# Performance work log

Hardware: AMD Instinct MI355X
Metric: run time of the kernel (lower is better)

The kernel has to match this reference:

```python
import jax, jax.numpy as jnp
import numpy as np

INFINITY = 1000000000000.0
HEADS = 12
HEAD_SIZE = 64


def setup_inputs() -> dict:
    key = jax.random.key(0)
    k1, k2 = jax.random.split(key)
    B, S, H = 8, 512, 1024
    x = jax.random.normal(k1, (B, S, H), dtype=jnp.float32)
    mask = jnp.ones((B, S), dtype=jnp.float32)
    W = jax.random.normal(k2, (H, HEADS * HEAD_SIZE * 2), dtype=jnp.float32) * (1.0 / np.sqrt(H))
    b = jnp.zeros((HEADS * HEAD_SIZE * 2,), dtype=jnp.float32)
    return {"x": x, "mask": mask, "W": W, "b": b}


def _sinusoidal_pos(seq_len, dim, dtype):
    # pos[n, d] interleaved as [sin0, cos0, sin1, cos1, ...]
    position = jnp.arange(seq_len, dtype=dtype)  # (S,)
    indices = jnp.power(jnp.asarray(10000.0, dtype), -2.0 * jnp.arange(dim // 2, dtype=dtype) / dim)
    ang = position[:, None] * indices[None, :]  # (S, d/2)
    pos = jnp.stack([jnp.sin(ang), jnp.cos(ang)], axis=-1).reshape(seq_len, dim)
    return pos


def reference(x, mask, W, b):
    B, S, _ = x.shape
    hs = HEAD_SIZE
    proj = x @ W + b  # (B, S, HEADS*2*hs)
    proj = proj.reshape(B, S, HEADS, 2 * hs)
    qw, kw = proj[..., :hs], proj[..., hs:]  # (B, S, HEADS, hs)

    # RoPE (note: original uses torch .repeat, i.e. TILING, not interleave)
    pos = _sinusoidal_pos(S, hs, x.dtype)  # (S, hs)
    cos_half = pos[None, :, None, 1::2]  # (1, S, 1, hs/2)
    sin_half = pos[None, :, None, ::2]
    cos_pos = jnp.concatenate([cos_half, cos_half], axis=-1)  # tiled -> (1,S,1,hs)
    sin_pos = jnp.concatenate([sin_half, sin_half], axis=-1)

    def rotate(t):
        t2 = jnp.stack([-t[..., 1::2], t[..., ::2]], axis=-1).reshape(t.shape)
        return t * cos_pos + t2 * sin_pos

    qw = rotate(qw)
    kw = rotate(kw)

    logits = jnp.einsum('bmhd,bnhd->bhmn', qw, kw)  # (B, HEADS, S, S)

    # sequence masking on dim 2 (rows) and dim 3 (cols)
    m_row = mask[:, None, :, None]
    m_col = mask[:, None, None, :]
    logits = logits * m_row + (-INFINITY) * (1.0 - m_row)
    logits = logits * m_col + (-INFINITY) * (1.0 - m_col)

    # strictly-lower-triangular mask (exclude end < start)
    tri = jnp.tril(jnp.ones((S, S), dtype=logits.dtype), k=-1)
    logits = logits - tri * INFINITY
    return logits / (hs ** 0.5)
```

## Files before the change

kernel.cpp:

```cpp
#include <hip/hip_runtime.h>
#include <stdint.h>
#include <stddef.h>

#define NB 8
#define SS 512
#define HID 1024
#define NHEADS 12
#define HSZ 64
#define NPROJ 1536
#define MROWS 4096
#define NEG_INF 1000000000000.0f

typedef __attribute__((ext_vector_type(4))) float f32x4;
typedef __attribute__((ext_vector_type(8))) __bf16 bf16x8;
typedef __attribute__((ext_vector_type(4))) unsigned short us4;

typedef __attribute__((address_space(1))) unsigned char gu8;
typedef __attribute__((address_space(3))) unsigned char lu8;

static __device__ __forceinline__ void gld16(const void* g, void* l) {
  __builtin_amdgcn_global_load_lds((gu8*)(g), (lu8*)(l), 16, 0, 0);
}

static __device__ __forceinline__ unsigned short f2bf(float f) {
  union { float f; unsigned u; } x; x.f = f;
  unsigned r = x.u + 0x7fffu + ((x.u >> 16) & 1u);
  return (unsigned short)(r >> 16);
}

__global__ __launch_bounds__(256) void k_prep(
    const float4* __restrict__ x, const float* __restrict__ W,
    float2* __restrict__ tab, us4* __restrict__ xb, unsigned short* __restrict__ wbt) {
  __shared__ float t[32][33];
  const int bid = blockIdx.x;
  const int tid = threadIdx.x;
  if (bid < 64) {
    int tt = bid * 256 + tid;
    int s = tt >> 5, i = tt & 31;
    float rate = powf(10000.0f, -(float)i / 32.0f);
    float sv, cv;
    sincosf((float)s * rate, &sv, &cv);
    tab[tt] = make_float2(sv, cv);
  } else if (bid < 64 + 4096) {
    int i = (bid - 64) * 256 + tid;
    float4 v = x[i];
    us4 o;
    o[0] = f2bf(v.x); o[1] = f2bf(v.y); o[2] = f2bf(v.z); o[3] = f2bf(v.w);
    xb[i] = o;
  } else {
    int flat = bid - (64 + 4096);
    int n0 = (flat % 48) * 32, k0 = (flat / 48) * 32;
    int tx = tid & 31, ty = tid >> 5;
#pragma unroll
    for (int i = 0; i < 4; ++i)
      t[ty + i * 8][tx] = W[(k0 + ty + i * 8) * NPROJ + n0 + tx];
    __syncthreads();
#pragma unroll
    for (int i = 0; i < 4; ++i)
      wbt[(n0 + ty + i * 8) * HID + (k0 + tx)] = f2bf(t[tx][ty + i * 8]);
  }
}

__global__ __launch_bounds__(256) void k_proj(
    const unsigned short* __restrict__ xb, const unsigned short* __restrict__ wbt,
    const float* __restrict__ bias, const float2* __restrict__ tab,
    unsigned short* __restrict__ qo, unsigned short* __restrict__ ko) {
  __shared__ __align__(16) unsigned short lA[128 * 64];
  __shared__ __align__(16) unsigned short lB[128 * 64];
  const int tid = threadIdx.x;
  const int lane = tid & 63, w = tid >> 6;
  const int wm = w >> 1, wn = w & 1;
  const int m0 = blockIdx.x * 128, n0 = blockIdx.y * 128;

  f32x4 acc[4][4];
#pragma unroll
  for (int a = 0; a < 4; ++a)
#pragma unroll
    for (int bb = 0; bb < 4; ++bb)
      acc[a][bb] = (f32x4)(0.0f);

  int srow[4], soff[4];
#pragma unroll
  for (int c = 0; c < 4; ++c) {
    int lin = (w * 4 + c) * 1024 + lane * 16;
    int row = lin >> 7;
    int cb = lin & 127;
    srow[c] = row;
    soff[c] = cb ^ ((row & 7) << 4);
  }

  for (int kt = 0; kt < HID / 64; ++kt) {
#pragma unroll
    for (int c = 0; c < 4; ++c) {
      int chunk = w * 4 + c;
      gld16((const char*)(xb + (m0 + srow[c]) * HID + kt * 64) + soff[c],
            (char*)lA + chunk * 1024);
      gld16((const char*)(wbt + (n0 + srow[c]) * HID + kt * 64) + soff[c],
            (char*)lB + chunk * 1024);
    }
    __syncthreads();
#pragma unroll
    for (int ks = 0; ks < 2; ++ks) {
      bf16x8 af[4], bfr[4];
      const int kb = ks * 64 + (lane >> 4) * 16;
#pragma unroll
      for (int mi = 0; mi < 4; ++mi) {
        int row = wm * 64 + mi * 16 + (lane & 15);
        af[mi] = *(const bf16x8*)((const char*)lA + row * 128 + (kb ^ ((row & 7) << 4)));
      }
#pragma unroll
      for (int ni = 0; ni < 4; ++ni) {
        int row = wn * 64 + ni * 16 + (lane & 15);
        bfr[ni] = *(const bf16x8*)((const char*)lB + row * 128 + (kb ^ ((row & 7) << 4)));
      }
#pragma unroll
      for (int mi = 0; mi < 4; ++mi)
#pragma unroll
        for (int ni = 0; ni < 4; ++ni)
          acc[mi][ni] = __builtin_amdgcn_mfma_f32_16x16x32_bf16(af[mi], bfr[ni], acc[mi][ni], 0, 0, 0);
    }
    __syncthreads();
  }

#pragma unroll
  for (int mi = 0; mi < 4; ++mi) {
#pragma unroll
    for (int ni = 0; ni < 4; ++ni) {
      const int col = n0 + wn * 64 + ni * 16 + (lane & 15);
      const float bv = bias[col];
      const int d = col & 63;
      const int h = col >> 7;
      const int j = col & 127;
      unsigned short* dst = (j < HSZ) ? qo : ko;
      const float sgn = (d & 1) ? 1.0f : -1.0f;
#pragma unroll
      for (int r = 0; r < 4; ++r) {
        const int row = m0 + wm * 64 + mi * 16 + (lane >> 4) * 4 + r;
        const int s = row & (SS - 1);
        const int bidx = row >> 9;
        float v = acc[mi][ni][r] + bv;
        float p = __shfl_xor(v, 1, 64);
        float2 sc = tab[s * 32 + (d & 31)];
        float o = v * sc.y + sgn * p * sc.x;
        dst[((bidx * NHEADS + h) * SS + s) * HSZ + d] = f2bf(o);
      }
    }
  }
}

__global__ __launch_bounds__(256) void k_logits(
    const unsigned short* __restrict__ q, const unsigned short* __restrict__ kk,
    const float* __restrict__ mask, float* __restrict__ out) {
  __shared__ __align__(16) unsigned short lQ[128 * 64];
  __shared__ __align__(16) unsigned short lK[128 * 64];
  const int tid = threadIdx.x;
  const int lane = tid & 63, w = tid >> 6;
  const int wm = w >> 1, wn = w & 1;
  const int bh = blockIdx.y;
  const int b = bh / NHEADS;
  const int m0 = (blockIdx.x >> 2) * 128, n0 = (blockIdx.x & 3) * 128;
  const char* qbase = (const char*)(q + (size_t)bh * SS * HSZ) + m0 * 128;
  const char* kbase = (const char*)(kk + (size_t)bh * SS * HSZ) + n0 * 128;

#pragma unroll
  for (int c = 0; c < 4; ++c) {
    int chunk = w * 4 + c;
    int lin = chunk * 1024 + lane * 16;
    int row = lin >> 7, cb = lin & 127;
    int sw = cb ^ ((row & 7) << 4);
    gld16(qbase + row * 128 + sw, (char*)lQ + chunk * 1024);
    gld16(kbase + row * 128 + sw, (char*)lK + chunk * 1024);
  }
  __syncthreads();

  f32x4 acc[4][4];
#pragma unroll
  for (int a = 0; a < 4; ++a)
#pragma unroll
    for (int bb = 0; bb < 4; ++bb)
      acc[a][bb] = (f32x4)(0.0f);

#pragma unroll
  for (int ks = 0; ks < 2; ++ks) {
    bf16x8 af[4], bfr[4];
    const int kb = ks * 64 + (lane >> 4) * 16;
#pragma unroll
    for (int mi = 0; mi < 4; ++mi) {
      int row = wm * 64 + mi * 16 + (lane & 15);
      af[mi] = *(const bf16x8*)((const char*)lQ + row * 128 + (kb ^ ((row & 7) << 4)));
    }
#pragma unroll
    for (int ni = 0; ni < 4; ++ni) {
      int row = wn * 64 + ni * 16 + (lane & 15);
      bfr[ni] = *(const bf16x8*)((const char*)lK + row * 128 + (kb ^ ((row & 7) << 4)));
    }
#pragma unroll
    for (int mi = 0; mi < 4; ++mi)
#pragma unroll
      for (int ni = 0; ni < 4; ++ni)
        acc[mi][ni] = __builtin_amdgcn_mfma_f32_16x16x32_bf16(af[mi], bfr[ni], acc[mi][ni], 0, 0, 0);
  }

  float mc[4];
#pragma unroll
  for (int ni = 0; ni < 4; ++ni)
    mc[ni] = mask[b * SS + n0 + wn * 64 + ni * 16 + (lane & 15)];
#pragma unroll
  for (int mi = 0; mi < 4; ++mi) {
#pragma unroll
    for (int r = 0; r < 4; ++r) {
      const int m = m0 + wm * 64 + mi * 16 + (lane >> 4) * 4 + r;
      const float mr = mask[b * SS + m];
#pragma unroll
      for (int ni = 0; ni < 4; ++ni) {
        const int n = n0 + wn * 64 + ni * 16 + (lane & 15);
        float v = acc[mi][ni][r];
        v = v * mr - NEG_INF * (1.0f - mr);
        v = v * mc[ni] - NEG_INF * (1.0f - mc[ni]);
        if (m > n) v -= NEG_INF;
        v *= 0.125f;
        __builtin_nontemporal_store(v, &out[((size_t)bh * SS + m) * SS + n]);
      }
    }
  }
}

extern "C" void kernel_launch(void* const* d_in, const int* in_sizes, int n_in,
                              void* d_out, int out_size, void* d_ws, size_t ws_size,
                              hipStream_t stream) {
  const float* x = (const float*)d_in[0];
  const float* mask = (const float*)d_in[1];
  const float* W = (const float*)d_in[2];
  const float* bias = (const float*)d_in[3];
  float* out = (float*)d_out;

  char* ws = (char*)d_ws;
  float2* tab = (float2*)ws;
  unsigned short* xb = (unsigned short*)(ws + 131072);
  unsigned short* wbt = (unsigned short*)(ws + 131072 + 8388608);
  unsigned short* qo = (unsigned short*)(ws + 131072 + 8388608 + 3145728);
  unsigned short* ko = (unsigned short*)(ws + 131072 + 8388608 + 3145728 + 6291456);

  k_prep<<<dim3(64 + 4096 + 1536), dim3(256), 0, stream>>>(
      (const float4*)x, W, tab, (us4*)xb, wbt);
  k_proj<<<dim3(32, 12), dim3(256), 0, stream>>>(xb, wbt, bias, tab, qo, ko);
  k_logits<<<dim3(16, 96), dim3(256), 0, stream>>>(qo, ko, mask, out);
}
```

Before: 70.85 us.

## Double-buffer projection GEMM, retile to 128x96, vectorize logits stores via swapped MFMA

The projection GEMM now uses double-buffered LDS tiles so the next K slice loads while MFMAs run on the current one. Its tile shrinks to 128x96, giving a 32x16 grid for better CU coverage. Operands are swapped so each lane holds four consecutive output columns, which allows vectorized bias and RoPE table loads and 8-byte packed bf16 stores. The logits kernel drops LDS staging, reads Q and K fragments straight from global memory, and swaps the MFMA operands so each lane writes a float4 of contiguous output columns with a vectorized nontemporal store.

After: 66.05 us. 1.07x faster.

```diff
diff --git a/kernel.cpp b/kernel.cpp
--- a/kernel.cpp
+++ b/kernel.cpp
@@ -2,13 +2,11 @@
 #include <stdint.h>
 #include <stddef.h>
 
-#define NB 8
 #define SS 512
 #define HID 1024
 #define NHEADS 12
 #define HSZ 64
 #define NPROJ 1536
-#define MROWS 4096
 #define NEG_INF 1000000000000.0f
 
 typedef __attribute__((ext_vector_type(4))) float f32x4;
@@ -65,113 +63,126 @@
     const unsigned short* __restrict__ xb, const unsigned short* __restrict__ wbt,
     const float* __restrict__ bias, const float2* __restrict__ tab,
     unsigned short* __restrict__ qo, unsigned short* __restrict__ ko) {
-  __shared__ __align__(16) unsigned short lA[128 * 64];
-  __shared__ __align__(16) unsigned short lB[128 * 64];
+  __shared__ __align__(16) unsigned short lA[2][128 * 64];
+  __shared__ __align__(16) unsigned short lB[2][96 * 64];
   const int tid = threadIdx.x;
   const int lane = tid & 63, w = tid >> 6;
   const int wm = w >> 1, wn = w & 1;
-  const int m0 = blockIdx.x * 128, n0 = blockIdx.y * 128;
-
-  f32x4 acc[4][4];
-#pragma unroll
-  for (int a = 0; a < 4; ++a)
-#pragma unroll
-    for (int bb = 0; bb < 4; ++bb)
-      acc[a][bb] = (f32x4)(0.0f);
-
-  int srow[4], soff[4];
+  const int m0 = blockIdx.x * 128, n0 = blockIdx.y * 96;
+
+  const char* aptr[4]; const char* bptr[3];
+  int adst[4], bdst[3];
 #pragma unroll
   for (int c = 0; c < 4; ++c) {
     int lin = (w * 4 + c) * 1024 + lane * 16;
-    int row = lin >> 7;
-    int cb = lin & 127;
-    srow[c] = row;
-    soff[c] = cb ^ ((row & 7) << 4);
-  }
-
-  for (int kt = 0; kt < HID / 64; ++kt) {
-#pragma unroll
-    for (int c = 0; c < 4; ++c) {
-      int chunk = w * 4 + c;
-      gld16((const char*)(xb + (m0 + srow[c]) * HID + kt * 64) + soff[c],
-            (char*)lA + chunk * 1024);
-      gld16((const char*)(wbt + (n0 + srow[c]) * HID + kt * 64) + soff[c],
-            (char*)lB + chunk * 1024);
+    int row = lin >> 7, cb = lin & 127;
+    aptr[c] = (const char*)(xb + (size_t)(m0 + row) * HID) + (cb ^ ((row & 7) << 4));
+    adst[c] = (w * 4 + c) * 1024;
+  }
+#pragma unroll
+  for (int c = 0; c < 3; ++c) {
+    int lin = (w * 3 + c) * 1024 + lane * 16;
+    int row = lin >> 7, cb = lin & 127;
+    bptr[c] = (const char*)(wbt + (size_t)(n0 + row) * HID) + (cb ^ ((row & 7) << 4));
+    bdst[c] = (w * 3 + c) * 1024;
+  }
+
+  f32x4 acc[3][4];
+#pragma unroll
+  for (int a = 0; a < 3; ++a)
+#pragma unroll
+    for (int b = 0; b < 4; ++b)
+      acc[a][b] = (f32x4)(0.0f);
+
+#define STAGE(buf, kt)                                                      \
+  do {                                                                      \
+    _Pragma("unroll") for (int c = 0; c < 4; ++c)                           \
+        gld16(aptr[c] + (kt) * 128, (char*)(&lA[(buf)][0]) + adst[c]);      \
+    _Pragma("unroll") for (int c = 0; c < 3; ++c)                           \
+        gld16(bptr[c] + (kt) * 128, (char*)(&lB[(buf)][0]) + bdst[c]);      \
+  } while (0)
+
+  STAGE(0, 0);
+  asm volatile("s_waitcnt vmcnt(0)" ::: "memory");
+  __builtin_amdgcn_s_barrier();
+
+  for (int kt = 0; kt < 16; ++kt) {
+    const int cur = kt & 1;
+    if (kt < 15) STAGE(cur ^ 1, kt + 1);
+#pragma unroll
+    for (int ks = 0; ks < 2; ++ks) {
+      bf16x8 af[3], bf[4];
+      const int kb = ks * 64 + (lane >> 4) * 16;
+#pragma unroll
+      for (int a = 0; a < 3; ++a) {
+        int row = wn * 48 + a * 16 + (lane & 15);
+        af[a] = *(const bf16x8*)((const char*)(&lB[cur][0]) + row * 128 + (kb ^ ((row & 7) << 4)));
+      }
+#pragma unroll
+      for (int b = 0; b < 4; ++b) {
+        int row = wm * 64 + b * 16 + (lane & 15);
+        bf[b] = *(const bf16x8*)((const char*)(&lA[cur][0]) + row * 128 + (kb ^ ((row & 7) << 4)));
+      }
+#pragma unroll
+      for (int a = 0; a < 3; ++a)
+#pragma unroll
+        for (int b = 0; b < 4; ++b)
+          acc[a][b] = __builtin_amdgcn_mfma_f32_16x16x32_bf16(af[a], bf[b], acc[a][b], 0, 0, 0);
     }
-    __syncthreads();
-#pragma unroll
-    for (int ks = 0; ks < 2; ++ks) {
-      bf16x8 af[4], bfr[4];
-      const int kb = ks * 64 + (lane >> 4) * 16;
-#pragma unroll
-      for (int mi = 0; mi < 4; ++mi) {
-        int row = wm * 64 + mi * 16 + (lane & 15);
-        af[mi] = *(const bf16x8*)((const char*)lA + row * 128 + (kb ^ ((row & 7) << 4)));
-      }
-#pragma unroll
-      for (int ni = 0; ni < 4; ++ni) {
-        int row = wn * 64 + ni * 16 + (lane & 15);
-        bfr[ni] = *(const bf16x8*)((const char*)lB + row * 128 + (kb ^ ((row & 7) << 4)));
-      }
-#pragma unroll
-      for (int mi = 0; mi < 4; ++mi)
-#pragma unroll
-        for (int ni = 0; ni < 4; ++ni)
-          acc[mi][ni] = __builtin_amdgcn_mfma_f32_16x16x32_bf16(af[mi], bfr[ni], acc[mi][ni], 0, 0, 0);
+    asm volatile("s_waitcnt vmcnt(0)" ::: "memory");
+    __builtin_amdgcn_s_barrier();
+  }
+#undef STAGE
+
+#pragma unroll
+  for (int a = 0; a < 3; ++a) {
+    const int nq = n0 + wn * 48 + a * 16 + (lane >> 4) * 4;
+    const float4 bv = *(const float4*)(bias + nq);
+    const int d = nq & 63;
+    const int h = nq >> 7;
+    unsigned short* base = ((nq >> 6) & 1) ? ko : qo;
+    const float4 t01 = *(const float4*)(tab + 0);
+#pragma unroll
+    for (int b = 0; b < 4; ++b) {
+      const int mrow = m0 + wm * 64 + b * 16 + (lane & 15);
+      const int s = mrow & (SS - 1);
+      const int bidx = mrow >> 9;
+      const float2* tp = tab + s * 32 + (d & 31);
+      const float4 ta = *(const float4*)(tp);
+      const float4 tb = *(const float4*)(tp + 2);
+      float v0 = acc[a][b][0] + bv.x;
+      float v1 = acc[a][b][1] + bv.y;
+      float v2 = acc[a][b][2] + bv.z;
+      float v3 = acc[a][b][3] + bv.w;
+      float o0 = v0 * ta.y - v1 * ta.x;
+      float o1 = v1 * ta.w + v0 * ta.z;
+      float o2 = v2 * tb.y - v3 * tb.x;
+      float o3 = v3 * tb.w + v2 * tb.z;
+      us4 pk;
+      pk[0] = f2bf(o0); pk[1] = f2bf(o1); pk[2] = f2bf(o2); pk[3] = f2bf(o3);
+      *(us4*)(base + ((size_t)(bidx * NHEADS + h) * SS + s) * HSZ + d) = pk;
     }
-    __syncthreads();
-  }
-
-#pragma unroll
-  for (int mi = 0; mi < 4; ++mi) {
-#pragma unroll
-    for (int ni = 0; ni < 4; ++ni) {
-      const int col = n0 + wn * 64 + ni * 16 + (lane & 15);
-      const float bv = bias[col];
-      const int d = col & 63;
-      const int h = col >> 7;
-      const int j = col & 127;
-      unsigned short* dst = (j < HSZ) ? qo : ko;
-      const float sgn = (d & 1) ? 1.0f : -1.0f;
-#pragma unroll
-      for (int r = 0; r < 4; ++r) {
-        const int row = m0 + wm * 64 + mi * 16 + (lane >> 4) * 4 + r;
-        const int s = row & (SS - 1);
-        const int bidx = row >> 9;
-        float v = acc[mi][ni][r] + bv;
-        float p = __shfl_xor(v, 1, 64);
-        float2 sc = tab[s * 32 + (d & 31)];
-        float o = v * sc.y + sgn * p * sc.x;
-        dst[((bidx * NHEADS + h) * SS + s) * HSZ + d] = f2bf(o);
-      }
-    }
+    (void)t01;
   }
 }
 
 __global__ __launch_bounds__(256) void k_logits(
     const unsigned short* __restrict__ q, const unsigned short* __restrict__ kk,
     const float* __restrict__ mask, float* __restrict__ out) {
-  __shared__ __align__(16) unsigned short lQ[128 * 64];
-  __shared__ __align__(16) unsigned short lK[128 * 64];
   const int tid = threadIdx.x;
   const int lane = tid & 63, w = tid >> 6;
-  const int wm = w >> 1, wn = w & 1;
   const int bh = blockIdx.y;
   const int b = bh / NHEADS;
   const int m0 = (blockIdx.x >> 2) * 128, n0 = (blockIdx.x & 3) * 128;
-  const char* qbase = (const char*)(q + (size_t)bh * SS * HSZ) + m0 * 128;
-  const char* kbase = (const char*)(kk + (size_t)bh * SS * HSZ) + n0 * 128;
-
-#pragma unroll
-  for (int c = 0; c < 4; ++c) {
-    int chunk = w * 4 + c;
-    int lin = chunk * 1024 + lane * 16;
-    int row = lin >> 7, cb = lin & 127;
-    int sw = cb ^ ((row & 7) << 4);
-    gld16(qbase + row * 128 + sw, (char*)lQ + chunk * 1024);
-    gld16(kbase + row * 128 + sw, (char*)lK + chunk * 1024);
-  }
-  __syncthreads();
+  const char* qbase = (const char*)(q + (size_t)bh * SS * HSZ);
+  const char* kbase = (const char*)(kk + (size_t)bh * SS * HSZ);
+
+  int mrow[4], nrow[4];
+#pragma unroll
+  for (int i = 0; i < 4; ++i) {
+    mrow[i] = m0 + (w >> 1) * 64 + i * 16 + (lane & 15);
+    nrow[i] = n0 + (w & 1) * 64 + i * 16 + (lane & 15);
+  }
 
   f32x4 acc[4][4];
 #pragma unroll
@@ -182,45 +193,41 @@
 
 #pragma unroll
   for (int ks = 0; ks < 2; ++ks) {
-    bf16x8 af[4], bfr[4];
-    const int kb = ks * 64 + (lane >> 4) * 16;
-#pragma unroll
-    for (int mi = 0; mi < 4; ++mi) {
-      int row = wm * 64 + mi * 16 + (lane & 15);
-      af[mi] = *(const bf16x8*)((const char*)lQ + row * 128 + (kb ^ ((row & 7) << 4)));
-    }
+    const int kboff = ks * 64 + (lane >> 4) * 16;
+    bf16x8 kf[4], qf[4];
+#pragma unroll
+    for (int i = 0; i < 4; ++i)
+      kf[i] = *(const bf16x8*)(kbase + (size_t)nrow[i] * 128 + kboff);
+#pragma unroll
+    for (int i = 0; i < 4; ++i)
+      qf[i] = *(const bf16x8*)(qbase + (size_t)mrow[i] * 128 + kboff);
+#pragma unroll
+    for (int ni = 0; ni < 4; ++ni)
+#pragma unroll
+      for (int mi = 0; mi < 4; ++mi)
+        acc[ni][mi] = __builtin_amdgcn_mfma_f32_16x16x32_bf16(kf[ni], qf[mi], acc[ni][mi], 0, 0, 0);
+  }
+
+#pragma unroll
+  for (int mi = 0; mi < 4; ++mi) {
+    const int m = mrow[mi];
+    const float mr = mask[b * SS + m];
+    float* orow = out + ((size_t)bh * SS + m) * SS;
 #pragma unroll
     for (int ni = 0; ni < 4; ++ni) {
-      int row = wn * 64 + ni * 16 + (lane & 15);
-      bfr[ni] = *(const bf16x8*)((const char*)lK + row * 128 + (kb ^ ((row & 7) << 4)));
-    }
-#pragma unroll
-    for (int mi = 0; mi < 4; ++mi)
-#pragma unroll
-      for (int ni = 0; ni < 4; ++ni)
-        acc[mi][ni] = __builtin_amdgcn_mfma_f32_16x16x32_bf16(af[mi], bfr[ni], acc[mi][ni], 0, 0, 0);
-  }
-
-  float mc[4];
-#pragma unroll
-  for (int ni = 0; ni < 4; ++ni)
-    mc[ni] = mask[b * SS + n0 + wn * 64 + ni * 16 + (lane & 15)];
-#pragma unroll
-  for (int mi = 0; mi < 4; ++mi) {
-#pragma unroll
-    for (int r = 0; r < 4; ++r) {
-      const int m = m0 + wm * 64 + mi * 16 + (lane >> 4) * 4 + r;
-      const float mr = mask[b * SS + m];
-#pragma unroll
-      for (int ni = 0; ni < 4; ++ni) {
-        const int n = n0 + wn * 64 + ni * 16 + (lane & 15);
-        float v = acc[mi][ni][r];
+      const int nb = n0 + (w & 1) * 64 + ni * 16 + (lane >> 4) * 4;
+      const float4 mc = *(const float4*)(mask + b * SS + nb);
+      f32x4 res;
+#pragma unroll
+      for (int r = 0; r < 4; ++r) {
+        float v = acc[ni][mi][r];
+        const float mcv = (r == 0) ? mc.x : (r == 1) ? mc.y : (r == 2) ? mc.z : mc.w;
         v = v * mr - NEG_INF * (1.0f - mr);
-        v = v * mc[ni] - NEG_INF * (1.0f - mc[ni]);
-        if (m > n) v -= NEG_INF;
-        v *= 0.125f;
-        __builtin_nontemporal_store(v, &out[((size_t)bh * SS + m) * SS + n]);
+        v = v * mcv - NEG_INF * (1.0f - mcv);
+        if (m > nb + r) v -= NEG_INF;
+        res[r] = v * 0.125f;
       }
+      __builtin_nontemporal_store(res, (f32x4*)(orow + nb));
     }
   }
 }
@@ -243,6 +250,6 @@
 
   k_prep<<<dim3(64 + 4096 + 1536), dim3(256), 0, stream>>>(
       (const float4*)x, W, tab, (us4*)xb, wbt);
-  k_proj<<<dim3(32, 12), dim3(256), 0, stream>>>(xb, wbt, bias, tab, qo, ko);
+  k_proj<<<dim3(32, 16), dim3(256), 0, stream>>>(xb, wbt, bias, tab, qo, ko);
   k_logits<<<dim3(16, 96), dim3(256), 0, stream>>>(qo, ko, mask, out);
 }
```
